# Kernel optimization log

Measured on AMD Instinct MI355X. Metric: run time of the kernel, lower is better.

Reference implementation:

```python
import jax, jax.numpy as jnp
import numpy as np

B, S, D, P = 4, 2048, 1024, 1024

def setup_inputs() -> dict:
    key = jax.random.key(0)
    k1, k2, k3, k4 = jax.random.split(key, 4)
    x = jax.random.normal(k1, (B, S, D), dtype=jnp.float32)
    # nn.Linear weight is (out, in); store transposed (in, out) for x @ W
    scale = 1.0 / np.sqrt(D)
    Wq = jax.random.normal(k2, (D, P), dtype=jnp.float32) * scale
    Wk = jax.random.normal(k3, (D, P), dtype=jnp.float32) * scale
    Wv = jax.random.normal(k4, (D, P), dtype=jnp.float32) * scale
    return {"x": x, "Wq": Wq, "Wk": Wk, "Wv": Wv}

def reference(x, Wq, Wk, Wv):
    # projections (no bias)
    q = x @ Wq  # (B,S,P)
    k = x @ Wk
    v = x @ Wv
    scores = jnp.einsum('bsd,btd->bst', q, k)  # (B,S,S)
    seq = x.shape[1]
    causal = jnp.triu(jnp.ones((seq, seq), dtype=bool), k=1)
    scores = jnp.where(causal, -jnp.inf, scores)
    scores = scores / jnp.sqrt(jnp.asarray(P, dtype=scores.dtype))
    attn = jax.nn.softmax(scores, axis=-1)
    # dropout_prob=0.0 -> identity
    context = jnp.einsum('bst,btd->bsd', attn, v)  # (B,S,P)
    return context
```

## Files before the change

### kernel.cpp

```cpp
#include <hip/hip_runtime.h>
#include <hip/hip_bf16.h>


#define BDIM 4
#define SDIM 2048
#define DDIM 1024
#define PDIM 1024

typedef __attribute__((ext_vector_type(8))) short bf16x8;
typedef __attribute__((ext_vector_type(4))) float f32x4;

__device__ __forceinline__ unsigned short f2bf(float f) {
    union { float f; unsigned int u; } v; v.f = f;
    unsigned int u = v.u;
    unsigned int r = (u + 0x7fffu + ((u >> 16) & 1u)) >> 16;
    return (unsigned short)r;
}

__device__ __forceinline__ float bf2f(unsigned short h) {
    union { unsigned int u; float f; } v;
    v.u = ((unsigned int)h) << 16;
    return v.f;
}

__device__ __forceinline__ void async16(const unsigned short* g, unsigned short* l) {
    __builtin_amdgcn_global_load_lds(
        (const __attribute__((address_space(1))) unsigned int*)g,
        (__attribute__((address_space(3))) unsigned int*)l,
        16, 0, 0);
}

__device__ __forceinline__ void storeC(float* C, size_t idx, float v) { C[idx] = v; }
__device__ __forceinline__ void storeC(unsigned short* C, size_t idx, float v) { C[idx] = f2bf(v); }

__global__ __launch_bounds__(256) void prep_kernel(const float* __restrict__ x,
                                                   const float* __restrict__ W0,
                                                   const float* __restrict__ W1,
                                                   const float* __restrict__ W2,
                                                   unsigned short* __restrict__ Xb,
                                                   unsigned short* __restrict__ WT) {
    int bid = blockIdx.x;
    if (bid < 4096) {
        size_t i = (size_t)bid * 256 + threadIdx.x;
        float4 a = ((const float4*)x)[2 * i];
        float4 b = ((const float4*)x)[2 * i + 1];
        bf16x8 o;
        o[0] = (short)f2bf(a.x); o[1] = (short)f2bf(a.y);
        o[2] = (short)f2bf(a.z); o[3] = (short)f2bf(a.w);
        o[4] = (short)f2bf(b.x); o[5] = (short)f2bf(b.y);
        o[6] = (short)f2bf(b.z); o[7] = (short)f2bf(b.w);
        ((bf16x8*)Xb)[i] = o;
    } else {
        int idx = bid - 4096;
        int wz = idx >> 10;
        int t = idx & 1023;
        const float* W = (wz == 0) ? W0 : (wz == 1) ? W1 : W2;
        unsigned short* Tz = WT + (size_t)wz * DDIM * PDIM;
        __shared__ float tle[32][33];
        int c0 = (t & 31) * 32, r0 = (t >> 5) * 32;
        int tx = threadIdx.x & 31, ty = threadIdx.x >> 5;
        for (int i = ty; i < 32; i += 8)
            tle[i][tx] = W[(size_t)(r0 + i) * PDIM + c0 + tx];
        __syncthreads();
        for (int i = ty; i < 32; i += 8)
            Tz[(size_t)(c0 + i) * DDIM + r0 + tx] = f2bf(tle[tx][i]);
    }
}

template <int LDA, int LDB, int LDC, int KMAX, int MODE, typename CT>
__global__ __launch_bounds__(256) void gemm_bt(
    const unsigned short* __restrict__ A0, const unsigned short* __restrict__ A1,
    long long sA,
    const unsigned short* __restrict__ B0, long long sB,
    CT* __restrict__ C0, CT* __restrict__ C1, long long sC,
    unsigned short* __restrict__ Kb, unsigned short* __restrict__ VT,
    float alpha) {
    const int BM = 128, BN = 128, BK = 64;
    const int BUF = BM * BK + BN * BK;
    __shared__ __attribute__((aligned(16))) unsigned short smem[2 * BUF];

    int tm, tn;
    if (MODE == 1) {
        int i = blockIdx.x;
        int t = (int)((sqrtf(8.f * i + 1.f) - 1.f) * 0.5f);
        if ((t + 1) * (t + 2) / 2 <= i) t++;
        if (t * (t + 1) / 2 > i) t--;
        tm = t * BM;
        tn = (i - t * (t + 1) / 2) * BN;
    } else {
        tm = blockIdx.y * BM;
        tn = blockIdx.x * BN;
    }
    int kend = (MODE == 2) ? min(KMAX, tm + BM) : KMAX;

    int z = blockIdx.z;
    const unsigned short* A = (z < 2 ? A0 : A1) + (long long)(z & 1) * sA;
    const unsigned short* Bt = B0 + (long long)z * sB;
    CT* C = (z < 2 ? C0 : C1) + (long long)(z & 1) * sC;

    int tid  = threadIdx.x;
    int lane = tid & 63;
    int wave = tid >> 6;
    int wr   = (wave >> 1) * 64;
    int wc   = (wave & 1) * 64;
    int quad = lane >> 4;
    int l16  = lane & 15;
    int rsw  = l16 & 7;

    f32x4 acc[4][4] = {};

    int srow = tid >> 3;
    int scol = ((tid & 7) ^ (srow & 7)) * 8;
    const unsigned short* Ag = A + (size_t)(tm + srow) * LDA + scol;
    const unsigned short* Bg = Bt + (size_t)(tn + srow) * LDB + scol;

    auto issue = [&](int k0, int buf) {
        unsigned short* la = smem + buf * BUF + tid * 8;
        unsigned short* lb = la + BM * BK;
        async16(Ag + k0, la);
        async16(Ag + k0 + 32 * LDA, la + 2048);
        async16(Ag + k0 + 64 * LDA, la + 4096);
        async16(Ag + k0 + 96 * LDA, la + 6144);
        async16(Bg + k0, lb);
        async16(Bg + k0 + 32 * LDB, lb + 2048);
        async16(Bg + k0 + 64 * LDB, lb + 4096);
        async16(Bg + k0 + 96 * LDB, lb + 6144);
    };

    auto compute = [&](int buf) {
        const unsigned short* As = smem + buf * BUF;
        const unsigned short* Bs = As + BM * BK;
#pragma unroll
        for (int s = 0; s < 2; s++) {
            int chunk = ((s * 4 + quad) ^ rsw) * 8;
            bf16x8 af[4], bfr[4];
#pragma unroll
            for (int i = 0; i < 4; i++)
                af[i] = *(const bf16x8*)(As + (wr + i * 16 + l16) * BK + chunk);
#pragma unroll
            for (int j = 0; j < 4; j++)
                bfr[j] = *(const bf16x8*)(Bs + (wc + j * 16 + l16) * BK + chunk);
#pragma unroll
            for (int i = 0; i < 4; i++)
#pragma unroll
                for (int j = 0; j < 4; j++)
                    acc[i][j] = __builtin_amdgcn_mfma_f32_16x16x32_bf16(af[i], bfr[j], acc[i][j], 0, 0, 0);
        }
    };

    if constexpr (MODE != 2) {
        constexpr int NS = KMAX / BK;
        issue(0, 0);
#pragma unroll
        for (int i = 0; i < NS; i++) {
            __syncthreads();
            if (i + 1 < NS) issue((i + 1) * BK, (i + 1) & 1);
            compute(i & 1);
        }
    } else {
        int ns = kend / BK;
        issue(0, 0);
        for (int i = 0; i < ns; i++) {
            __syncthreads();
            if (i + 1 < ns) issue((i + 1) * BK, (i + 1) & 1);
            compute(i & 1);
        }
    }

    if constexpr (MODE == 0) {
        if (tn < 2048) {
            unsigned short* D = (tn < 1024 ? (unsigned short*)C0 : Kb);
            int cbase = tn & 1023;
#pragma unroll
            for (int i = 0; i < 4; i++) {
                int r0 = tm + wr + i * 16 + quad * 4;
#pragma unroll
                for (int j = 0; j < 4; j++) {
                    int c = cbase + wc + j * 16 + l16;
#pragma unroll
                    for (int rr = 0; rr < 4; rr++)
                        D[(size_t)(r0 + rr) * 1024 + c] = f2bf(acc[i][j][rr]);
                }
            }
        } else {
            int b = tm >> 11;
            int s0 = tm & 2047;
            unsigned short* VTb = VT + (size_t)b * (PDIM * SDIM)
                                     + (size_t)(tn - 2048) * SDIM + s0;
            const int TP = 136;
            unsigned short* T = smem;
            __syncthreads();
#pragma unroll
            for (int p = 0; p < 4; p++) {
                int jbase = -1;
                if (wc == 0 && p == 0) jbase = 0;
                if (wc == 0 && p == 1) jbase = 2;
                if (wc == 64 && p == 2) jbase = 0;
                if (wc == 64 && p == 3) jbase = 2;
                if (jbase >= 0) {
#pragma unroll
                    for (int jj = 0; jj < 2; jj++) {
                        int j = jbase + jj;
                        int c = (wc + j * 16 + l16) - 32 * p;
#pragma unroll
                        for (int i = 0; i < 4; i++) {
                            int r = wr + i * 16 + quad * 4;
                            ushort4 w;
                            w.x = f2bf(acc[i][j][0]); w.y = f2bf(acc[i][j][1]);
                            w.z = f2bf(acc[i][j][2]); w.w = f2bf(acc[i][j][3]);
                            *(ushort4*)(T + c * TP + r) = w;
                        }
                    }
                }
                __syncthreads();
                {
                    int lr = tid >> 3;
                    int ck = (tid & 7) * 16;
                    bf16x8 u0 = *(const bf16x8*)(T + lr * TP + ck);
                    bf16x8 u1 = *(const bf16x8*)(T + lr * TP + ck + 8);
                    unsigned short* dst = VTb + (size_t)(32 * p + lr) * SDIM + ck;
                    *(bf16x8*)(dst) = u0;
                    *(bf16x8*)(dst + 8) = u1;
                }
                __syncthreads();
            }
        }
    } else {
#pragma unroll
        for (int i = 0; i < 4; i++) {
            int r0 = tm + wr + i * 16 + quad * 4;
#pragma unroll
            for (int j = 0; j < 4; j++) {
                int c = tn + wc + j * 16 + l16;
#pragma unroll
                for (int rr = 0; rr < 4; rr++) {
                    int r = r0 + rr;
                    if (MODE == 1 && c > r) continue;
                    storeC(C, (size_t)r * LDC + c, acc[i][j][rr] * alpha);
                }
            }
        }
    }
}

__global__ __launch_bounds__(256) void softmax_causal(unsigned short* __restrict__ S01,
                                                      unsigned short* __restrict__ S23,
                                                      long long sS) {
    int row = blockIdx.x;
    int b = blockIdx.y;
    unsigned short* srow = (b < 2 ? S01 : S23) + (long long)(b & 1) * sS + (size_t)row * SDIM;
    int tid = threadIdx.x;
    int j0 = tid * 8;
    int valid = row + 1;
    int bound = ((row >> 7) + 1) << 7;
    bool active = j0 < valid;
    __shared__ float red[4];

    float f[8];
    if (active) {
        bf16x8 v8 = *(const bf16x8*)(srow + j0);
#pragma unroll
        for (int i = 0; i < 8; i++) f[i] = bf2f((unsigned short)v8[i]);
    }

    float m = -1e30f;
    if (active) {
#pragma unroll
        for (int i = 0; i < 8; i++) if (j0 + i < valid) m = fmaxf(m, f[i]);
    }
#pragma unroll
    for (int o = 32; o; o >>= 1) m = fmaxf(m, __shfl_xor(m, o, 64));
    if ((tid & 63) == 0) red[tid >> 6] = m;
    __syncthreads();
    m = fmaxf(fmaxf(red[0], red[1]), fmaxf(red[2], red[3]));
    __syncthreads();

    float e[8] = {0.f, 0.f, 0.f, 0.f, 0.f, 0.f, 0.f, 0.f};
    float l = 0.f;
    if (active) {
#pragma unroll
        for (int i = 0; i < 8; i++) {
            e[i] = (j0 + i < valid) ? __expf(f[i] - m) : 0.f;
            l += e[i];
        }
    }
#pragma unroll
    for (int o = 32; o; o >>= 1) l += __shfl_xor(l, o, 64);
    if ((tid & 63) == 0) red[tid >> 6] = l;
    __syncthreads();
    l = red[0] + red[1] + red[2] + red[3];
    float inv = 1.0f / l;

    if (j0 < bound) {
        bf16x8 o8;
#pragma unroll
        for (int i = 0; i < 8; i++) o8[i] = (short)f2bf(e[i] * inv);
        *(bf16x8*)(srow + j0) = o8;
    }
}

extern "C" void kernel_launch(void* const* d_in, const int* in_sizes, int n_in,
                              void* d_out, int out_size, void* d_ws, size_t ws_size,
                              hipStream_t stream) {
    const float* x  = (const float*)d_in[0];
    const float* Wq = (const float*)d_in[1];
    const float* Wk = (const float*)d_in[2];
    const float* Wv = (const float*)d_in[3];
    float* out = (float*)d_out;

    const size_t MS = (size_t)BDIM * SDIM;
    const long long SS = (long long)SDIM * SDIM;
    char* ws = (char*)d_ws;
    size_t off = 0;
    unsigned short* Xb   = (unsigned short*)(ws + off);
    unsigned short* S01  = Xb;                          off += MS * DDIM * 2;
    unsigned short* WT   = (unsigned short*)(ws + off); off += 3ull * DDIM * PDIM * 2;
    unsigned short* Q    = (unsigned short*)(ws + off); off += MS * PDIM * 2;
    unsigned short* Kb   = (unsigned short*)(ws + off); off += MS * PDIM * 2;
    unsigned short* VT   = (unsigned short*)(ws + off); off += MS * PDIM * 2;
    unsigned short* S23  = (unsigned short*)(ws + off); off += 2ull * SS * 2;

    prep_kernel<<<4096 + 3072, 256, 0, stream>>>(x, Wq, Wk, Wv, Xb, WT);

    gemm_bt<DDIM, DDIM, PDIM, DDIM, 0, unsigned short>
        <<<dim3(3 * PDIM / 128, MS / 128, 1), 256, 0, stream>>>(
        Xb, Xb, 0, WT, 0, Q, Q, 0, Kb, VT, 1.0f);

    const long long sQ = (long long)SDIM * PDIM;
    const float alpha = 1.0f / 32.0f;

    gemm_bt<PDIM, PDIM, SDIM, PDIM, 1, unsigned short>
        <<<dim3(136, 1, BDIM), 256, 0, stream>>>(
        Q, Q + 2 * sQ, sQ, Kb, sQ, S01, S23, SS, nullptr, nullptr, alpha);

    softmax_causal<<<dim3(SDIM, BDIM), 256, 0, stream>>>(S01, S23, SS);

    const long long sOut = (long long)SDIM * PDIM;
    gemm_bt<SDIM, SDIM, PDIM, SDIM, 2, float>
        <<<dim3(PDIM / 128, SDIM / 128, BDIM), 256, 0, stream>>>(
        S01, S23, SS, VT, sQ, out, out + 2 * sOut, sOut, nullptr, nullptr, 1.0f);
}
```

Before: 232.5 us.

## Load B operand fragments directly from global into registers, bypassing LDS

```diff
diff --git a/kernel.cpp b/kernel.cpp
--- a/kernel.cpp
+++ b/kernel.cpp
@@ -76,8 +76,8 @@
     unsigned short* __restrict__ Kb, unsigned short* __restrict__ VT,
     float alpha) {
     const int BM = 128, BN = 128, BK = 64;
-    const int BUF = BM * BK + BN * BK;
-    __shared__ __attribute__((aligned(16))) unsigned short smem[2 * BUF];
+    const int ABUF = BM * BK;
+    __shared__ __attribute__((aligned(16))) unsigned short smem[2 * ABUF];
 
     int tm, tn;
     if (MODE == 1) {
@@ -112,58 +112,66 @@
     int srow = tid >> 3;
     int scol = ((tid & 7) ^ (srow & 7)) * 8;
     const unsigned short* Ag = A + (size_t)(tm + srow) * LDA + scol;
-    const unsigned short* Bg = Bt + (size_t)(tn + srow) * LDB + scol;
-
-    auto issue = [&](int k0, int buf) {
-        unsigned short* la = smem + buf * BUF + tid * 8;
-        unsigned short* lb = la + BM * BK;
+    const unsigned short* Bg = Bt + (size_t)(tn + wc + l16) * LDB + quad * 8;
+
+    auto issueA = [&](int k0, int buf) {
+        unsigned short* la = smem + buf * ABUF + tid * 8;
         async16(Ag + k0, la);
         async16(Ag + k0 + 32 * LDA, la + 2048);
         async16(Ag + k0 + 64 * LDA, la + 4096);
         async16(Ag + k0 + 96 * LDA, la + 6144);
-        async16(Bg + k0, lb);
-        async16(Bg + k0 + 32 * LDB, lb + 2048);
-        async16(Bg + k0 + 64 * LDB, lb + 4096);
-        async16(Bg + k0 + 96 * LDB, lb + 6144);
     };
 
-    auto compute = [&](int buf) {
-        const unsigned short* As = smem + buf * BUF;
-        const unsigned short* Bs = As + BM * BK;
+    bf16x8 bb[2][2][4];
+
+    auto loadB = [&](int buf, int k0) {
+#pragma unroll
+        for (int s = 0; s < 2; s++)
+#pragma unroll
+            for (int j = 0; j < 4; j++)
+                bb[buf][s][j] = *(const bf16x8*)(Bg + (size_t)j * 16 * LDB + k0 + s * 32);
+    };
+
+    auto compute = [&](int abuf, int bbuf) {
+        const unsigned short* As = smem + abuf * ABUF;
 #pragma unroll
         for (int s = 0; s < 2; s++) {
             int chunk = ((s * 4 + quad) ^ rsw) * 8;
-            bf16x8 af[4], bfr[4];
+            bf16x8 af[4];
 #pragma unroll
             for (int i = 0; i < 4; i++)
                 af[i] = *(const bf16x8*)(As + (wr + i * 16 + l16) * BK + chunk);
 #pragma unroll
-            for (int j = 0; j < 4; j++)
-                bfr[j] = *(const bf16x8*)(Bs + (wc + j * 16 + l16) * BK + chunk);
-#pragma unroll
             for (int i = 0; i < 4; i++)
 #pragma unroll
                 for (int j = 0; j < 4; j++)
-                    acc[i][j] = __builtin_amdgcn_mfma_f32_16x16x32_bf16(af[i], bfr[j], acc[i][j], 0, 0, 0);
+                    acc[i][j] = __builtin_amdgcn_mfma_f32_16x16x32_bf16(
+                        af[i], bb[bbuf][s][j], acc[i][j], 0, 0, 0);
         }
     };
 
     if constexpr (MODE != 2) {
         constexpr int NS = KMAX / BK;
-        issue(0, 0);
+        issueA(0, 0);
+        loadB(0, 0);
 #pragma unroll
         for (int i = 0; i < NS; i++) {
             __syncthreads();
-            if (i + 1 < NS) issue((i + 1) * BK, (i + 1) & 1);
-            compute(i & 1);
+            if (i + 1 < NS) { issueA((i + 1) * BK, (i + 1) & 1); loadB((i + 1) & 1, (i + 1) * BK); }
+            compute(i & 1, i & 1);
         }
     } else {
         int ns = kend / BK;
-        issue(0, 0);
-        for (int i = 0; i < ns; i++) {
+        issueA(0, 0);
+        loadB(0, 0);
+        for (int i = 0; i < ns; i += 2) {
             __syncthreads();
-            if (i + 1 < ns) issue((i + 1) * BK, (i + 1) & 1);
-            compute(i & 1);
+            issueA((i + 1) * BK, 1);
+            loadB(1, (i + 1) * BK);
+            compute(0, 0);
+            __syncthreads();
+            if (i + 2 < ns) { issueA((i + 2) * BK, 0); loadB(0, (i + 2) * BK); }
+            compute(1, 1);
         }
     }
 
```

Result: slower. 346.8 us (+49.2%).
